# Performance work log

Hardware: AMD Instinct MI355X
Metric: run time of the kernel (lower is better)

The kernel has to match this reference:

```python
import jax, jax.numpy as jnp
import numpy as np

B, S, D, H, F = 64, 512, 1024, 1024, 1024  # note: module requires H == D
EPS = 1e-6


def setup_inputs() -> dict:
    key = jax.random.key(0)
    ks = jax.random.split(key, 14)
    p = lambda k, shape: 0.02 * jax.random.normal(k, shape, dtype=jnp.float32)
    return {
        "hidden_state": jax.random.normal(ks[0], (B, S, D), dtype=jnp.float32),
        "field_hidden_state": jax.random.normal(ks[1], (B, S, F), dtype=jnp.float32),
        "input": jax.random.normal(ks[2], (B, D), dtype=jnp.float32),
        "finished": jnp.zeros((B, 1), dtype=bool),
        "W1": p(ks[3], (H, D)), "b1": p(ks[4], (H,)),
        "W2": p(ks[5], (H, D)), "b2": p(ks[6], (H,)),
        "W3": p(ks[7], (H, 2 * D)), "b3": p(ks[8], (H,)),
        "W4": p(ks[9], (H, F)), "b4": p(ks[10], (H,)),
        "W5": p(ks[11], (H, D)), "b5": p(ks[12], (H,)),
    }


def _norm_over_seq(w):
    # manual exp/max/sum softmax over seq dim (axis 0) with 1e-6 guard, as in torch
    w = jnp.exp(w - jnp.max(w, axis=0, keepdims=True))
    return w / (EPS + jnp.sum(w, axis=0, keepdims=True))


def reference(hidden_state, field_hidden_state, input, finished,
              W1, b1, W2, b2, W3, b3, W4, b4, W5, b5):
    hs = jnp.transpose(hidden_state, (1, 0, 2))        # [S, B, D]
    fs = jnp.transpose(field_hidden_state, (1, 0, 2))  # [S, B, F]
    phi_h = jnp.tanh(hs @ W1.T + b1)                   # [S, B, H]
    phi_f = jnp.tanh(fs @ W4.T + b4)                   # [S, B, H]

    gamma_h = jnp.tanh(input @ W2.T + b2)              # [B, H]
    weights = _norm_over_seq(jnp.sum(phi_h * gamma_h, axis=2, keepdims=True))  # [S, B, 1]

    alpha_h = jnp.tanh(input @ W5.T + b5)              # [B, H]
    field_w = _norm_over_seq(jnp.sum(phi_f * alpha_h, axis=2, keepdims=True))  # [S, B, 1]

    wf = weights * field_w
    weights = wf / (EPS + jnp.sum(wf, axis=0, keepdims=True))  # [S, B, 1]

    context = jnp.sum(hs * weights, axis=0)            # [B, D]
    out = jnp.concatenate([context, input], axis=-1) @ W3.T + b3  # [B, H]
    out = jnp.where(finished, jnp.zeros_like(out), out)
    return out, weights
```

## Files before the change

### kernel.cpp

```cpp
#include <hip/hip_runtime.h>

#define EPS 1e-6f

typedef _Float16 f16;
typedef _Float16 f16x4 __attribute__((ext_vector_type(4)));
typedef _Float16 f16x8 __attribute__((ext_vector_type(8)));
typedef float f32x4 __attribute__((ext_vector_type(4)));

__device__ __forceinline__ float tanh_fast(float x) {
    float e = __expf(2.0f * x);
    return 1.0f - 2.0f / (e + 1.0f);
}

__global__ __launch_bounds__(256) void conv_kernel(
    const float4* __restrict__ src, f16x4* __restrict__ dst, int n4)
{
    int stride = gridDim.x * 256;
    for (int i = blockIdx.x * 256 + threadIdx.x; i < n4; i += stride) {
        float4 v = src[i];
        f16x4 o; o[0]=(f16)v.x; o[1]=(f16)v.y; o[2]=(f16)v.z; o[3]=(f16)v.w;
        dst[i] = o;
    }
}

__global__ __launch_bounds__(256) void gamal_kernel(
    const float* __restrict__ inp,
    const float* __restrict__ W2, const float* __restrict__ b2,
    const float* __restrict__ W5, const float* __restrict__ b5,
    float* __restrict__ gamm, float* __restrict__ alph)
{
    const float* W  = blockIdx.y ? W5 : W2;
    const float* bs = blockIdx.y ? b5 : b2;
    float* dst      = blockIdx.y ? alph : gamm;
    int wid = threadIdx.x >> 6, lane = threadIdx.x & 63;
    int p = blockIdx.x * 4 + wid;
    int b = p >> 10, h = p & 1023;
    const float4* wr = (const float4*)(W + (size_t)h * 1024);
    const float4* xr = (const float4*)(inp + (size_t)b * 1024);
    float acc = 0.f;
    #pragma unroll
    for (int j = 0; j < 4; ++j) {
        float4 w4 = wr[lane + 64 * j];
        float4 x4 = xr[lane + 64 * j];
        acc += w4.x * x4.x + w4.y * x4.y + w4.z * x4.z + w4.w * x4.w;
    }
    #pragma unroll
    for (int o = 32; o; o >>= 1) acc += __shfl_xor(acc, o);
    if (lane == 0) dst[p] = tanh_fast(acc + bs[h]);
}

__global__ __launch_bounds__(256, 4) void gemm_logits_kernel(
    const f16* __restrict__ Ah,
    const f16* __restrict__ Wh,
    const float* __restrict__ b1, const float* __restrict__ b4,
    const float* __restrict__ gamm, const float* __restrict__ alph,
    float* __restrict__ Lpart)
{
    __shared__ __align__(16) char smA[16384];
    __shared__ __align__(16) char smW[16384];
    __shared__ float rowpart[128][2];

    const int lin = blockIdx.x;
    const int gidx = (lin & 7) * 512 + (lin >> 3);
    const int mat = gidx >> 11;
    const int rem = gidx & 2047;
    const int m_blk = rem >> 3;
    const int nc = rem & 7;
    const int m0 = m_blk << 7;
    const int hc0 = nc << 7;
    const int bidx = m_blk >> 2;

    const f16* A   = Ah + (size_t)mat * 33554432;
    const f16* W   = Wh + (size_t)mat * 1048576;
    const float* bv = mat ? b4 : b1;
    const float* gv = mat ? alph : gamm;

    const int t = threadIdx.x;
    const int lane = t & 63;
    const int wv = t >> 6;
    const int wr = wv >> 1;
    const int wc = wv & 1;
    const int c16 = lane & 15;
    const int kg = lane >> 4;

    const int lrow = lane >> 3, lslot = lane & 7;
    const int kchunk = lslot ^ lrow;

    const int swzr = (c16 & 7) << 4;
    const int aoffb = (wr * 64 + c16) * 128;
    const int woffb = (wc * 64 + c16) * 128;
    const int kg16 = kg * 16;

    f32x4 acc[4][4];
    #pragma unroll
    for (int i = 0; i < 4; ++i)
        #pragma unroll
        for (int j = 0; j < 4; ++j) acc[i][j] = (f32x4){0.f, 0.f, 0.f, 0.f};

    for (int kt = 0; kt < 16; ++kt) {
        #pragma unroll
        for (int j = 0; j < 4; ++j) {
            int r = wv * 32 + j * 8;
            const f16* srcA = A + (size_t)(m0 + r + lrow) * 1024 + kt * 64 + kchunk * 8;
            __builtin_amdgcn_global_load_lds(
                (const __attribute__((address_space(1))) void*)srcA,
                (__attribute__((address_space(3))) void*)(smA + r * 128), 16, 0, 0);
        }
        #pragma unroll
        for (int j = 0; j < 4; ++j) {
            int r = wv * 32 + j * 8;
            const f16* srcW = W + (size_t)(hc0 + r + lrow) * 1024 + kt * 64 + kchunk * 8;
            __builtin_amdgcn_global_load_lds(
                (const __attribute__((address_space(1))) void*)srcW,
                (__attribute__((address_space(3))) void*)(smW + r * 128), 16, 0, 0);
        }
        __syncthreads();

        #pragma unroll
        for (int kk = 0; kk < 2; ++kk) {
            const int ko = (kk * 64 + kg16) ^ swzr;
            f16x8 af[4], wf[4];
            #pragma unroll
            for (int i = 0; i < 4; ++i) af[i] = *(const f16x8*)(smA + aoffb + i * 2048 + ko);
            #pragma unroll
            for (int i = 0; i < 4; ++i) wf[i] = *(const f16x8*)(smW + woffb + i * 2048 + ko);
            #pragma unroll
            for (int ni = 0; ni < 4; ++ni)
                #pragma unroll
                for (int mi = 0; mi < 4; ++mi)
                    acc[mi][ni] = __builtin_amdgcn_mfma_f32_16x16x32_f16(af[mi], wf[ni], acc[mi][ni], 0, 0, 0);
        }
        __syncthreads();
    }

    float g[4], bb[4];
    #pragma unroll
    for (int ni = 0; ni < 4; ++ni) {
        int h = hc0 + wc * 64 + ni * 16 + c16;
        g[ni]  = gv[(bidx << 10) + h];
        bb[ni] = bv[h];
    }
    #pragma unroll
    for (int mi = 0; mi < 4; ++mi) {
        #pragma unroll
        for (int q = 0; q < 4; ++q) {
            float v = tanh_fast(acc[mi][0][q] + bb[0]) * g[0]
                    + tanh_fast(acc[mi][1][q] + bb[1]) * g[1]
                    + tanh_fast(acc[mi][2][q] + bb[2]) * g[2]
                    + tanh_fast(acc[mi][3][q] + bb[3]) * g[3];
            v += __shfl_xor(v, 1);
            v += __shfl_xor(v, 2);
            v += __shfl_xor(v, 4);
            v += __shfl_xor(v, 8);
            if (c16 == 0)
                rowpart[wr * 64 + mi * 16 + kg * 4 + q][wc] = v;
        }
    }
    __syncthreads();
    if (t < 128)
        Lpart[(size_t)(mat * 8 + nc) * 32768 + m0 + t] = rowpart[t][0] + rowpart[t][1];
}

__device__ __forceinline__ float blockMax(float v, float* sm) {
    #pragma unroll
    for (int o = 32; o; o >>= 1) v = fmaxf(v, __shfl_xor(v, o));
    if ((threadIdx.x & 63) == 0) sm[threadIdx.x >> 6] = v;
    __syncthreads();
    v = fmaxf(fmaxf(sm[0], sm[1]), fmaxf(sm[2], sm[3]));
    __syncthreads();
    return v;
}
__device__ __forceinline__ float blockSum(float v, float* sm) {
    #pragma unroll
    for (int o = 32; o; o >>= 1) v += __shfl_xor(v, o);
    if ((threadIdx.x & 63) == 0) sm[threadIdx.x >> 6] = v;
    __syncthreads();
    v = sm[0] + sm[1] + sm[2] + sm[3];
    __syncthreads();
    return v;
}

__global__ __launch_bounds__(256) void softmax_combine_kernel(
    const float* __restrict__ Lp,
    float* __restrict__ wfin, float* __restrict__ dout)
{
    __shared__ float sm[4];
    int b = blockIdx.x, t = threadIdx.x;
    float h0 = 0.f, h1 = 0.f, f0 = 0.f, f1 = 0.f;
    #pragma unroll
    for (int nc = 0; nc < 8; ++nc) {
        h0 += Lp[nc * 32768 + b * 512 + t];
        h1 += Lp[nc * 32768 + b * 512 + 256 + t];
        f0 += Lp[(8 + nc) * 32768 + b * 512 + t];
        f1 += Lp[(8 + nc) * 32768 + b * 512 + 256 + t];
    }
    float mh = blockMax(fmaxf(h0, h1), sm);
    float mf = blockMax(fmaxf(f0, f1), sm);
    float e0 = __expf(h0 - mh), e1 = __expf(h1 - mh);
    float q0 = __expf(f0 - mf), q1 = __expf(f1 - mf);
    float sh = blockSum(e0 + e1, sm);
    float sf = blockSum(q0 + q1, sm);
    float wh0 = e0 / (EPS + sh), wh1 = e1 / (EPS + sh);
    float wq0 = q0 / (EPS + sf), wq1 = q1 / (EPS + sf);
    float c0 = wh0 * wq0, c1 = wh1 * wq1;
    float sc = blockSum(c0 + c1, sm);
    float r0 = c0 / (EPS + sc), r1 = c1 / (EPS + sc);
    wfin[b * 512 + t]       = r0;
    wfin[b * 512 + 256 + t] = r1;
    dout[65536 + t * 64 + b]         = r0;
    dout[65536 + (256 + t) * 64 + b] = r1;
}

__global__ __launch_bounds__(256) void context_kernel(
    const f16* __restrict__ Ah, const float* __restrict__ wgt,
    float* __restrict__ ctxpart)
{
    int dq = blockIdx.x;
    int b  = blockIdx.y;
    int sh = blockIdx.z;
    int t = threadIdx.x;
    int ss = t >> 6, ds = t & 63;
    __shared__ float part[4][64][8];
    float a[8] = {0,0,0,0,0,0,0,0};
    int sBase = sh * 256 + ss * 64;
    const f16* hp = Ah + (size_t)b * 524288 + dq * 512 + ds * 8;
    for (int i = 0; i < 64; ++i) {
        int s = sBase + i;
        float w = wgt[b * 512 + s];
        f16x8 v = *(const f16x8*)(hp + (size_t)s * 1024);
        #pragma unroll
        for (int j = 0; j < 8; ++j) a[j] += w * (float)v[j];
    }
    #pragma unroll
    for (int j = 0; j < 8; ++j) part[ss][ds][j] = a[j];
    __syncthreads();
    if (ss == 0) {
        #pragma unroll
        for (int j = 0; j < 8; ++j) {
            float o = part[0][ds][j] + part[1][ds][j] + part[2][ds][j] + part[3][ds][j];
            ctxpart[(size_t)sh * 65536 + b * 1024 + dq * 512 + ds * 8 + j] = o;
        }
    }
}

__global__ __launch_bounds__(256) void out_kernel(
    const float* __restrict__ ctxpart, const float* __restrict__ inp,
    const float* __restrict__ W3, const float* __restrict__ b3,
    const unsigned char* __restrict__ fin, float* __restrict__ out)
{
    int t = threadIdx.x, wid = t >> 6, lane = t & 63;
    int h = blockIdx.x * 4 + wid;
    __shared__ __align__(16) float xs[2048];
    float4* xsv = (float4*)xs;
    float4 wreg[8];
    const float4* w3r = (const float4*)(W3 + (size_t)h * 2048);
    #pragma unroll
    for (int j = 0; j < 8; ++j) wreg[j] = w3r[lane + 64 * j];
    const float4* cp = (const float4*)ctxpart;
    const float4* xp = (const float4*)inp;
    for (int b = 0; b < 64; ++b) {
        __syncthreads();
        {
            float4 c0 = cp[b * 256 + t];
            float4 c1 = cp[16384 + b * 256 + t];
            float4 cc; cc.x = c0.x + c1.x; cc.y = c0.y + c1.y;
            cc.z = c0.z + c1.z; cc.w = c0.w + c1.w;
            xsv[t] = cc;
            xsv[256 + t] = xp[b * 256 + t];
        }
        __syncthreads();
        float acc = 0.f;
        #pragma unroll
        for (int j = 0; j < 8; ++j) {
            float4 x = xsv[lane + 64 * j];
            acc += wreg[j].x * x.x + wreg[j].y * x.y + wreg[j].z * x.z + wreg[j].w * x.w;
        }
        #pragma unroll
        for (int o = 32; o; o >>= 1) acc += __shfl_xor(acc, o);
        if (lane == 0) out[b * 1024 + h] = fin[b] ? 0.f : (acc + b3[h]);
    }
}

extern "C" void kernel_launch(void* const* d_in, const int* in_sizes, int n_in,
                              void* d_out, int out_size, void* d_ws, size_t ws_size,
                              hipStream_t stream)
{
    const float* hidden = (const float*)d_in[0];
    const float* field  = (const float*)d_in[1];
    const float* input  = (const float*)d_in[2];
    const unsigned char* fin = (const unsigned char*)d_in[3];
    const float* W1 = (const float*)d_in[4];
    const float* b1 = (const float*)d_in[5];
    const float* W2 = (const float*)d_in[6];
    const float* b2 = (const float*)d_in[7];
    const float* W3 = (const float*)d_in[8];
    const float* b3 = (const float*)d_in[9];
    const float* W4 = (const float*)d_in[10];
    const float* b4 = (const float*)d_in[11];
    const float* W5 = (const float*)d_in[12];
    const float* b5 = (const float*)d_in[13];
    float* out = (float*)d_out;

    char* ws = (char*)d_ws;
    float* Lpart = (float*)(ws);
    float* wfin  = (float*)(ws + 2097152);
    float* gamm  = (float*)(ws + 2228224);
    float* alph  = (float*)(ws + 2490368);
    float* ctxp  = (float*)(ws + 2752512);
    f16*   Wh    = (f16*)(ws + 3276800);
    f16*   Ah    = (f16*)(ws + 7471104);

    conv_kernel<<<4096, 256, 0, stream>>>((const float4*)hidden, (f16x4*)Ah, 8388608);
    conv_kernel<<<4096, 256, 0, stream>>>((const float4*)field,  (f16x4*)(Ah + 33554432), 8388608);
    conv_kernel<<<1024, 256, 0, stream>>>((const float4*)W1, (f16x4*)Wh, 262144);
    conv_kernel<<<1024, 256, 0, stream>>>((const float4*)W4, (f16x4*)(Wh + 1048576), 262144);

    gamal_kernel<<<dim3(16384, 2), 256, 0, stream>>>(input, W2, b2, W5, b5, gamm, alph);
    gemm_logits_kernel<<<4096, 256, 0, stream>>>(Ah, Wh, b1, b4, gamm, alph, Lpart);
    softmax_combine_kernel<<<64, 256, 0, stream>>>(Lpart, wfin, out);
    context_kernel<<<dim3(2, 64, 2), 256, 0, stream>>>(Ah, wfin, ctxp);
    out_kernel<<<256, 256, 0, stream>>>(ctxp, input, W3, b3, fin, out);
}
```

Baseline: 344.3 us.

## Rework logits GEMM into 256x256 tiles with double-buffered phased LDS pipeline

The logits GEMM moves from 128x128 tiles with 4 waves to 256x256 tiles with 8 waves, using double-buffered LDS (128 KB) and a four-phase schedule. Each phase issues global-to-LDS loads for the next k-tile while running MFMAs on the current one, separated by raw s_barrier, sched_barrier and setprio hints. The larger tile halves the number of column-chunk partials written and summed by the softmax kernel, and raises operand reuse per LDS byte. The costs are occupancy limited to one block per CU, heavy register pressure from 32 accumulators, and fragile manual vmcnt accounting.

```diff
diff --git a/kernel.cpp b/kernel.cpp
--- a/kernel.cpp
+++ b/kernel.cpp
@@ -6,6 +6,10 @@
 typedef _Float16 f16x4 __attribute__((ext_vector_type(4)));
 typedef _Float16 f16x8 __attribute__((ext_vector_type(8)));
 typedef float f32x4 __attribute__((ext_vector_type(4)));
+
+#define PHASE_BAR() do { __builtin_amdgcn_sched_barrier(0); \
+                         __builtin_amdgcn_s_barrier();      \
+                         __builtin_amdgcn_sched_barrier(0); } while (0)
 
 __device__ __forceinline__ float tanh_fast(float x) {
     float e = __expf(2.0f * x);
@@ -49,37 +53,37 @@
     if (lane == 0) dst[p] = tanh_fast(acc + bs[h]);
 }
 
-__global__ __launch_bounds__(256, 4) void gemm_logits_kernel(
+__global__ __launch_bounds__(512, 1) void gemm_logits_kernel(
     const f16* __restrict__ Ah,
     const f16* __restrict__ Wh,
     const float* __restrict__ b1, const float* __restrict__ b4,
     const float* __restrict__ gamm, const float* __restrict__ alph,
     float* __restrict__ Lpart)
 {
-    __shared__ __align__(16) char smA[16384];
-    __shared__ __align__(16) char smW[16384];
-    __shared__ float rowpart[128][2];
+    __shared__ __align__(16) char smA[2][32768];
+    __shared__ __align__(16) char smW[2][32768];
+    __shared__ float rowpart[256][4];
 
     const int lin = blockIdx.x;
-    const int gidx = (lin & 7) * 512 + (lin >> 3);
-    const int mat = gidx >> 11;
-    const int rem = gidx & 2047;
-    const int m_blk = rem >> 3;
-    const int nc = rem & 7;
-    const int m0 = m_blk << 7;
-    const int hc0 = nc << 7;
-    const int bidx = m_blk >> 2;
-
-    const f16* A   = Ah + (size_t)mat * 33554432;
-    const f16* W   = Wh + (size_t)mat * 1048576;
+    const int swz = (lin & 7) * 128 + (lin >> 3);
+    const int mat = swz >> 9;
+    const int rem = swz & 511;
+    const int m_blk = rem >> 2;
+    const int nc = rem & 3;
+    const int m0 = m_blk << 8;
+    const int hc0 = nc << 8;
+    const int bidx = m_blk >> 1;
+
+    const f16* A = Ah + (size_t)mat * 33554432;
+    const f16* W = Wh + (size_t)mat * 1048576;
     const float* bv = mat ? b4 : b1;
     const float* gv = mat ? alph : gamm;
 
     const int t = threadIdx.x;
     const int lane = t & 63;
     const int wv = t >> 6;
-    const int wr = wv >> 1;
-    const int wc = wv & 1;
+    const int wr = wv >> 2;
+    const int wc = wv & 3;
     const int c16 = lane & 15;
     const int kg = lane >> 4;
 
@@ -87,50 +91,126 @@
     const int kchunk = lslot ^ lrow;
 
     const int swzr = (c16 & 7) << 4;
-    const int aoffb = (wr * 64 + c16) * 128;
+    const int aoffb = (wr * 128 + c16) * 128;
     const int woffb = (wc * 64 + c16) * 128;
     const int kg16 = kg * 16;
 
-    f32x4 acc[4][4];
-    #pragma unroll
-    for (int i = 0; i < 4; ++i)
+    f32x4 acc[8][4];
+    #pragma unroll
+    for (int i = 0; i < 8; ++i)
         #pragma unroll
         for (int j = 0; j < 4; ++j) acc[i][j] = (f32x4){0.f, 0.f, 0.f, 0.f};
 
+    auto stageA = [&](int kt, char* buf, int h) {
+        #pragma unroll
+        for (int j = 0; j < 2; ++j) {
+            int q = wv * 2 + j;
+            int r = (q >> 3) * 128 + h * 64 + (q & 7) * 8;
+            const f16* src = A + (size_t)(m0 + r + lrow) * 1024 + kt * 64 + kchunk * 8;
+            __builtin_amdgcn_global_load_lds(
+                (const __attribute__((address_space(1))) void*)src,
+                (__attribute__((address_space(3))) void*)(buf + r * 128), 16, 0, 0);
+        }
+    };
+    auto stageW = [&](int kt, char* buf, int h) {
+        #pragma unroll
+        for (int j = 0; j < 2; ++j) {
+            int q = wv * 2 + j;
+            int r = (q >> 2) * 64 + h * 32 + (q & 3) * 8;
+            const f16* src = W + (size_t)(hc0 + r + lrow) * 1024 + kt * 64 + kchunk * 8;
+            __builtin_amdgcn_global_load_lds(
+                (const __attribute__((address_space(1))) void*)src,
+                (__attribute__((address_space(3))) void*)(buf + r * 128), 16, 0, 0);
+        }
+    };
+
+    stageA(0, smA[0], 0); stageA(0, smA[0], 1);
+    stageW(0, smW[0], 0); stageW(0, smW[0], 1);
+    stageA(1, smA[1], 0);
+    __builtin_amdgcn_sched_barrier(0);
+    asm volatile("s_waitcnt vmcnt(2)" ::: "memory");
+    PHASE_BAR();
+
     for (int kt = 0; kt < 16; ++kt) {
-        #pragma unroll
-        for (int j = 0; j < 4; ++j) {
-            int r = wv * 32 + j * 8;
-            const f16* srcA = A + (size_t)(m0 + r + lrow) * 1024 + kt * 64 + kchunk * 8;
-            __builtin_amdgcn_global_load_lds(
-                (const __attribute__((address_space(1))) void*)srcA,
-                (__attribute__((address_space(3))) void*)(smA + r * 128), 16, 0, 0);
-        }
-        #pragma unroll
-        for (int j = 0; j < 4; ++j) {
-            int r = wv * 32 + j * 8;
-            const f16* srcW = W + (size_t)(hc0 + r + lrow) * 1024 + kt * 64 + kchunk * 8;
-            __builtin_amdgcn_global_load_lds(
-                (const __attribute__((address_space(1))) void*)srcW,
-                (__attribute__((address_space(3))) void*)(smW + r * 128), 16, 0, 0);
-        }
-        __syncthreads();
-
-        #pragma unroll
-        for (int kk = 0; kk < 2; ++kk) {
-            const int ko = (kk * 64 + kg16) ^ swzr;
-            f16x8 af[4], wf[4];
-            #pragma unroll
-            for (int i = 0; i < 4; ++i) af[i] = *(const f16x8*)(smA + aoffb + i * 2048 + ko);
-            #pragma unroll
-            for (int i = 0; i < 4; ++i) wf[i] = *(const f16x8*)(smW + woffb + i * 2048 + ko);
-            #pragma unroll
-            for (int ni = 0; ni < 4; ++ni)
+        char* aC = smA[kt & 1];
+        char* wC = smW[kt & 1];
+        char* aN = smA[(kt & 1) ^ 1];
+        char* wN = smW[(kt & 1) ^ 1];
+        const int kt1 = kt < 15 ? kt + 1 : 15;
+        const int kt2 = kt < 14 ? kt + 2 : 15;
+
+        f16x8 af[8], bf0[4], bf1[4];
+
+        stageA(kt1, aN, 1);
+        #pragma unroll
+        for (int mi = 0; mi < 4; ++mi)
+            #pragma unroll
+            for (int kk = 0; kk < 2; ++kk)
+                af[mi * 2 + kk] = *(const f16x8*)(aC + aoffb + mi * 2048 + ((kk * 64 + kg16) ^ swzr));
+        #pragma unroll
+        for (int ni = 0; ni < 2; ++ni)
+            #pragma unroll
+            for (int kk = 0; kk < 2; ++kk)
+                bf0[ni * 2 + kk] = *(const f16x8*)(wC + woffb + ni * 2048 + ((kk * 64 + kg16) ^ swzr));
+        __builtin_amdgcn_s_setprio(1);
+        #pragma unroll
+        for (int ni = 0; ni < 2; ++ni)
+            #pragma unroll
+            for (int mi = 0; mi < 4; ++mi)
                 #pragma unroll
-                for (int mi = 0; mi < 4; ++mi)
-                    acc[mi][ni] = __builtin_amdgcn_mfma_f32_16x16x32_f16(af[mi], wf[ni], acc[mi][ni], 0, 0, 0);
-        }
-        __syncthreads();
+                for (int kk = 0; kk < 2; ++kk)
+                    acc[mi][ni] = __builtin_amdgcn_mfma_f32_16x16x32_f16(af[mi * 2 + kk], bf0[ni * 2 + kk], acc[mi][ni], 0, 0, 0);
+        __builtin_amdgcn_s_setprio(0);
+        PHASE_BAR();
+
+        stageW(kt1, wN, 0);
+        #pragma unroll
+        for (int ni = 0; ni < 2; ++ni)
+            #pragma unroll
+            for (int kk = 0; kk < 2; ++kk)
+                bf1[ni * 2 + kk] = *(const f16x8*)(wC + woffb + 4096 + ni * 2048 + ((kk * 64 + kg16) ^ swzr));
+        __builtin_amdgcn_s_setprio(1);
+        #pragma unroll
+        for (int ni = 0; ni < 2; ++ni)
+            #pragma unroll
+            for (int mi = 0; mi < 4; ++mi)
+                #pragma unroll
+                for (int kk = 0; kk < 2; ++kk)
+                    acc[mi][ni + 2] = __builtin_amdgcn_mfma_f32_16x16x32_f16(af[mi * 2 + kk], bf1[ni * 2 + kk], acc[mi][ni + 2], 0, 0, 0);
+        __builtin_amdgcn_s_setprio(0);
+        PHASE_BAR();
+
+        stageW(kt1, wN, 1);
+        #pragma unroll
+        for (int mi = 0; mi < 4; ++mi)
+            #pragma unroll
+            for (int kk = 0; kk < 2; ++kk)
+                af[mi * 2 + kk] = *(const f16x8*)(aC + aoffb + 8192 + mi * 2048 + ((kk * 64 + kg16) ^ swzr));
+        __builtin_amdgcn_s_setprio(1);
+        #pragma unroll
+        for (int ni = 0; ni < 2; ++ni)
+            #pragma unroll
+            for (int mi = 0; mi < 4; ++mi)
+                #pragma unroll
+                for (int kk = 0; kk < 2; ++kk)
+                    acc[mi + 4][ni] = __builtin_amdgcn_mfma_f32_16x16x32_f16(af[mi * 2 + kk], bf0[ni * 2 + kk], acc[mi + 4][ni], 0, 0, 0);
+        __builtin_amdgcn_s_setprio(0);
+        PHASE_BAR();
+
+        stageA(kt2, aC, 0);
+        __builtin_amdgcn_sched_barrier(0);
+        __builtin_amdgcn_s_setprio(1);
+        #pragma unroll
+        for (int ni = 0; ni < 2; ++ni)
+            #pragma unroll
+            for (int mi = 0; mi < 4; ++mi)
+                #pragma unroll
+                for (int kk = 0; kk < 2; ++kk)
+                    acc[mi + 4][ni + 2] = __builtin_amdgcn_mfma_f32_16x16x32_f16(af[mi * 2 + kk], bf1[ni * 2 + kk], acc[mi + 4][ni + 2], 0, 0, 0);
+        __builtin_amdgcn_s_setprio(0);
+        __builtin_amdgcn_sched_barrier(0);
+        asm volatile("s_waitcnt vmcnt(2)" ::: "memory");
+        PHASE_BAR();
     }
 
     float g[4], bb[4];
@@ -141,7 +221,7 @@
         bb[ni] = bv[h];
     }
     #pragma unroll
-    for (int mi = 0; mi < 4; ++mi) {
+    for (int mi = 0; mi < 8; ++mi) {
         #pragma unroll
         for (int q = 0; q < 4; ++q) {
             float v = tanh_fast(acc[mi][0][q] + bb[0]) * g[0]
@@ -153,12 +233,13 @@
             v += __shfl_xor(v, 4);
             v += __shfl_xor(v, 8);
             if (c16 == 0)
-                rowpart[wr * 64 + mi * 16 + kg * 4 + q][wc] = v;
-        }
-    }
-    __syncthreads();
-    if (t < 128)
-        Lpart[(size_t)(mat * 8 + nc) * 32768 + m0 + t] = rowpart[t][0] + rowpart[t][1];
+                rowpart[wr * 128 + mi * 16 + kg * 4 + q][wc] = v;
+        }
+    }
+    __syncthreads();
+    if (t < 256)
+        Lpart[(size_t)(mat * 4 + nc) * 32768 + m0 + t] =
+            rowpart[t][0] + rowpart[t][1] + rowpart[t][2] + rowpart[t][3];
 }
 
 __device__ __forceinline__ float blockMax(float v, float* sm) {
@@ -188,11 +269,11 @@
     int b = blockIdx.x, t = threadIdx.x;
     float h0 = 0.f, h1 = 0.f, f0 = 0.f, f1 = 0.f;
     #pragma unroll
-    for (int nc = 0; nc < 8; ++nc) {
+    for (int nc = 0; nc < 4; ++nc) {
         h0 += Lp[nc * 32768 + b * 512 + t];
         h1 += Lp[nc * 32768 + b * 512 + 256 + t];
-        f0 += Lp[(8 + nc) * 32768 + b * 512 + t];
-        f1 += Lp[(8 + nc) * 32768 + b * 512 + 256 + t];
+        f0 += Lp[(4 + nc) * 32768 + b * 512 + t];
+        f1 += Lp[(4 + nc) * 32768 + b * 512 + 256 + t];
     }
     float mh = blockMax(fmaxf(h0, h1), sm);
     float mf = blockMax(fmaxf(f0, f1), sm);
@@ -316,7 +397,7 @@
     conv_kernel<<<1024, 256, 0, stream>>>((const float4*)W4, (f16x4*)(Wh + 1048576), 262144);
 
     gamal_kernel<<<dim3(16384, 2), 256, 0, stream>>>(input, W2, b2, W5, b5, gamm, alph);
-    gemm_logits_kernel<<<4096, 256, 0, stream>>>(Ah, Wh, b1, b4, gamm, alph, Lpart);
+    gemm_logits_kernel<<<1024, 512, 0, stream>>>(Ah, Wh, b1, b4, gamm, alph, Lpart);
     softmax_combine_kernel<<<64, 256, 0, stream>>>(Lpart, wfin, out);
     context_kernel<<<dim3(2, 64, 2), 256, 0, stream>>>(Ah, wfin, ctxp);
     out_kernel<<<256, 256, 0, stream>>>(ctxp, input, W3, b3, fin, out);
```

New measurement: 365.3 us. 1.06x slower.

## Widen logits GEMM tile to 128x256 and fuse fp16 conversion launches

Applied to the files above, without the earlier changes.

Merges the four fp32-to-fp16 conversion launches into one grid-stride kernel that picks its source buffer by index range. The logits GEMM tile grows from 128x128 to 128x256, so each wave holds 4x8 accumulators, the A tile is reloaded half as often, and only 4 N-chunk partials are written, with the softmax reduction updated to match. In exchange the kernel uses more registers and LDS, and its launch bound drops from 4 to 2 blocks per CU, which lowers occupancy and latency hiding.

```diff
diff --git a/kernel.cpp b/kernel.cpp
--- a/kernel.cpp
+++ b/kernel.cpp
@@ -12,14 +12,22 @@
     return 1.0f - 2.0f / (e + 1.0f);
 }
 
-__global__ __launch_bounds__(256) void conv_kernel(
-    const float4* __restrict__ src, f16x4* __restrict__ dst, int n4)
-{
-    int stride = gridDim.x * 256;
-    for (int i = blockIdx.x * 256 + threadIdx.x; i < n4; i += stride) {
-        float4 v = src[i];
+__global__ __launch_bounds__(256) void convall_kernel(
+    const float4* __restrict__ hidden, const float4* __restrict__ field,
+    const float4* __restrict__ W1, const float4* __restrict__ W4,
+    f16x4* __restrict__ Ah, f16x4* __restrict__ Af,
+    f16x4* __restrict__ Wh1, f16x4* __restrict__ Wh4)
+{
+    const int stride = gridDim.x * 256;
+    for (int i = blockIdx.x * 256 + threadIdx.x; i < 17301504; i += stride) {
+        const float4* s; f16x4* d; int off;
+        if (i < 8388608)       { s = hidden; d = Ah;  off = i; }
+        else if (i < 16777216) { s = field;  d = Af;  off = i - 8388608; }
+        else if (i < 17039360) { s = W1;     d = Wh1; off = i - 16777216; }
+        else                   { s = W4;     d = Wh4; off = i - 17039360; }
+        float4 v = s[off];
         f16x4 o; o[0]=(f16)v.x; o[1]=(f16)v.y; o[2]=(f16)v.z; o[3]=(f16)v.w;
-        dst[i] = o;
+        d[off] = o;
     }
 }
 
@@ -49,7 +57,7 @@
     if (lane == 0) dst[p] = tanh_fast(acc + bs[h]);
 }
 
-__global__ __launch_bounds__(256, 4) void gemm_logits_kernel(
+__global__ __launch_bounds__(256, 2) void gemm_logits_kernel(
     const f16* __restrict__ Ah,
     const f16* __restrict__ Wh,
     const float* __restrict__ b1, const float* __restrict__ b4,
@@ -57,21 +65,21 @@
     float* __restrict__ Lpart)
 {
     __shared__ __align__(16) char smA[16384];
-    __shared__ __align__(16) char smW[16384];
+    __shared__ __align__(16) char smW[32768];
     __shared__ float rowpart[128][2];
 
     const int lin = blockIdx.x;
-    const int gidx = (lin & 7) * 512 + (lin >> 3);
-    const int mat = gidx >> 11;
-    const int rem = gidx & 2047;
-    const int m_blk = rem >> 3;
-    const int nc = rem & 7;
+    const int swz = (lin & 7) * 256 + (lin >> 3);
+    const int mat = swz >> 10;
+    const int rem = swz & 1023;
+    const int m_blk = rem >> 2;
+    const int nc = rem & 3;
     const int m0 = m_blk << 7;
-    const int hc0 = nc << 7;
+    const int hc0 = nc << 8;
     const int bidx = m_blk >> 2;
 
-    const f16* A   = Ah + (size_t)mat * 33554432;
-    const f16* W   = Wh + (size_t)mat * 1048576;
+    const f16* A = Ah + (size_t)mat * 33554432;
+    const f16* W = Wh + (size_t)mat * 1048576;
     const float* bv = mat ? b4 : b1;
     const float* gv = mat ? alph : gamm;
 
@@ -88,14 +96,14 @@
 
     const int swzr = (c16 & 7) << 4;
     const int aoffb = (wr * 64 + c16) * 128;
-    const int woffb = (wc * 64 + c16) * 128;
+    const int woffb = (wc * 128 + c16) * 128;
     const int kg16 = kg * 16;
 
-    f32x4 acc[4][4];
+    f32x4 acc[4][8];
     #pragma unroll
     for (int i = 0; i < 4; ++i)
         #pragma unroll
-        for (int j = 0; j < 4; ++j) acc[i][j] = (f32x4){0.f, 0.f, 0.f, 0.f};
+        for (int j = 0; j < 8; ++j) acc[i][j] = (f32x4){0.f, 0.f, 0.f, 0.f};
 
     for (int kt = 0; kt < 16; ++kt) {
         #pragma unroll
@@ -107,8 +115,8 @@
                 (__attribute__((address_space(3))) void*)(smA + r * 128), 16, 0, 0);
         }
         #pragma unroll
-        for (int j = 0; j < 4; ++j) {
-            int r = wv * 32 + j * 8;
+        for (int j = 0; j < 8; ++j) {
+            int r = wv * 64 + j * 8;
             const f16* srcW = W + (size_t)(hc0 + r + lrow) * 1024 + kt * 64 + kchunk * 8;
             __builtin_amdgcn_global_load_lds(
                 (const __attribute__((address_space(1))) void*)srcW,
@@ -119,13 +127,13 @@
         #pragma unroll
         for (int kk = 0; kk < 2; ++kk) {
             const int ko = (kk * 64 + kg16) ^ swzr;
-            f16x8 af[4], wf[4];
+            f16x8 af[4], wf[8];
             #pragma unroll
             for (int i = 0; i < 4; ++i) af[i] = *(const f16x8*)(smA + aoffb + i * 2048 + ko);
             #pragma unroll
-            for (int i = 0; i < 4; ++i) wf[i] = *(const f16x8*)(smW + woffb + i * 2048 + ko);
+            for (int i = 0; i < 8; ++i) wf[i] = *(const f16x8*)(smW + woffb + i * 2048 + ko);
             #pragma unroll
-            for (int ni = 0; ni < 4; ++ni)
+            for (int ni = 0; ni < 8; ++ni)
                 #pragma unroll
                 for (int mi = 0; mi < 4; ++mi)
                     acc[mi][ni] = __builtin_amdgcn_mfma_f32_16x16x32_f16(af[mi], wf[ni], acc[mi][ni], 0, 0, 0);
@@ -133,10 +141,10 @@
         __syncthreads();
     }
 
-    float g[4], bb[4];
-    #pragma unroll
-    for (int ni = 0; ni < 4; ++ni) {
-        int h = hc0 + wc * 64 + ni * 16 + c16;
+    float g[8], bb[8];
+    #pragma unroll
+    for (int ni = 0; ni < 8; ++ni) {
+        int h = hc0 + wc * 128 + ni * 16 + c16;
         g[ni]  = gv[(bidx << 10) + h];
         bb[ni] = bv[h];
     }
@@ -144,10 +152,10 @@
     for (int mi = 0; mi < 4; ++mi) {
         #pragma unroll
         for (int q = 0; q < 4; ++q) {
-            float v = tanh_fast(acc[mi][0][q] + bb[0]) * g[0]
-                    + tanh_fast(acc[mi][1][q] + bb[1]) * g[1]
-                    + tanh_fast(acc[mi][2][q] + bb[2]) * g[2]
-                    + tanh_fast(acc[mi][3][q] + bb[3]) * g[3];
+            float v = 0.f;
+            #pragma unroll
+            for (int ni = 0; ni < 8; ++ni)
+                v += tanh_fast(acc[mi][ni][q] + bb[ni]) * g[ni];
             v += __shfl_xor(v, 1);
             v += __shfl_xor(v, 2);
             v += __shfl_xor(v, 4);
@@ -158,7 +166,7 @@
     }
     __syncthreads();
     if (t < 128)
-        Lpart[(size_t)(mat * 8 + nc) * 32768 + m0 + t] = rowpart[t][0] + rowpart[t][1];
+        Lpart[(size_t)(mat * 4 + nc) * 32768 + m0 + t] = rowpart[t][0] + rowpart[t][1];
 }
 
 __device__ __forceinline__ float blockMax(float v, float* sm) {
@@ -188,11 +196,11 @@
     int b = blockIdx.x, t = threadIdx.x;
     float h0 = 0.f, h1 = 0.f, f0 = 0.f, f1 = 0.f;
     #pragma unroll
-    for (int nc = 0; nc < 8; ++nc) {
+    for (int nc = 0; nc < 4; ++nc) {
         h0 += Lp[nc * 32768 + b * 512 + t];
         h1 += Lp[nc * 32768 + b * 512 + 256 + t];
-        f0 += Lp[(8 + nc) * 32768 + b * 512 + t];
-        f1 += Lp[(8 + nc) * 32768 + b * 512 + 256 + t];
+        f0 += Lp[(4 + nc) * 32768 + b * 512 + t];
+        f1 += Lp[(4 + nc) * 32768 + b * 512 + 256 + t];
     }
     float mh = blockMax(fmaxf(h0, h1), sm);
     float mf = blockMax(fmaxf(f0, f1), sm);
@@ -310,13 +318,14 @@
     f16*   Wh    = (f16*)(ws + 3276800);
     f16*   Ah    = (f16*)(ws + 7471104);
 
-    conv_kernel<<<4096, 256, 0, stream>>>((const float4*)hidden, (f16x4*)Ah, 8388608);
-    conv_kernel<<<4096, 256, 0, stream>>>((const float4*)field,  (f16x4*)(Ah + 33554432), 8388608);
-    conv_kernel<<<1024, 256, 0, stream>>>((const float4*)W1, (f16x4*)Wh, 262144);
-    conv_kernel<<<1024, 256, 0, stream>>>((const float4*)W4, (f16x4*)(Wh + 1048576), 262144);
+    convall_kernel<<<8192, 256, 0, stream>>>(
+        (const float4*)hidden, (const float4*)field,
+        (const float4*)W1, (const float4*)W4,
+        (f16x4*)Ah, (f16x4*)(Ah + 33554432),
+        (f16x4*)Wh, (f16x4*)(Wh + 1048576));
 
     gamal_kernel<<<dim3(16384, 2), 256, 0, stream>>>(input, W2, b2, W5, b5, gamm, alph);
-    gemm_logits_kernel<<<4096, 256, 0, stream>>>(Ah, Wh, b1, b4, gamm, alph, Lpart);
+    gemm_logits_kernel<<<2048, 256, 0, stream>>>(Ah, Wh, b1, b4, gamm, alph, Lpart);
     softmax_combine_kernel<<<64, 256, 0, stream>>>(Lpart, wfin, out);
     context_kernel<<<dim3(2, 64, 2), 256, 0, stream>>>(Ah, wfin, ctxp);
     out_kernel<<<256, 256, 0, stream>>>(ctxp, input, W3, b3, fin, out);
```

Result: faster. 327.8 us (-4.8%).

## Fuse fp32-to-fp16 activation conversion into GEMM A-tile loading

Applied to the files above, without the earlier changes.

Drops the separate conversion passes over hidden and field states. The logits GEMM now loads fp32 activations into registers, converts them with packed round-toward-zero conversion and writes them swizzled into LDS, prefetching the next K tile. The context kernel reads fp32 hidden directly. The gamma/alpha kernel reuses each weight row across 8 batch rows, and the weight conversions are merged into one launch. This removes a large extra write and read of the activations, at the cost of more register pressure (occupancy hint lowered to 3) and doubled global read bytes for A inside the GEMM.

```diff
diff --git a/kernel.cpp b/kernel.cpp
--- a/kernel.cpp
+++ b/kernel.cpp
@@ -3,6 +3,7 @@
 #define EPS 1e-6f
 
 typedef _Float16 f16;
+typedef __fp16 h16x2 __attribute__((ext_vector_type(2)));
 typedef _Float16 f16x4 __attribute__((ext_vector_type(4)));
 typedef _Float16 f16x8 __attribute__((ext_vector_type(8)));
 typedef float f32x4 __attribute__((ext_vector_type(4)));
@@ -12,14 +13,18 @@
     return 1.0f - 2.0f / (e + 1.0f);
 }
 
-__global__ __launch_bounds__(256) void conv_kernel(
-    const float4* __restrict__ src, f16x4* __restrict__ dst, int n4)
-{
-    int stride = gridDim.x * 256;
-    for (int i = blockIdx.x * 256 + threadIdx.x; i < n4; i += stride) {
-        float4 v = src[i];
+__global__ __launch_bounds__(256) void convw_kernel(
+    const float4* __restrict__ W1, const float4* __restrict__ W4,
+    f16x4* __restrict__ Wh1, f16x4* __restrict__ Wh4)
+{
+    const int stride = gridDim.x * 256;
+    for (int i = blockIdx.x * 256 + threadIdx.x; i < 524288; i += stride) {
+        const float4* s = (i < 262144) ? W1 : W4;
+        f16x4* d       = (i < 262144) ? Wh1 : Wh4;
+        int off = i & 262143;
+        float4 v = s[off];
         f16x4 o; o[0]=(f16)v.x; o[1]=(f16)v.y; o[2]=(f16)v.z; o[3]=(f16)v.w;
-        dst[i] = o;
+        d[off] = o;
     }
 }
 
@@ -33,24 +38,31 @@
     const float* bs = blockIdx.y ? b5 : b2;
     float* dst      = blockIdx.y ? alph : gamm;
     int wid = threadIdx.x >> 6, lane = threadIdx.x & 63;
-    int p = blockIdx.x * 4 + wid;
-    int b = p >> 10, h = p & 1023;
+    int hb = blockIdx.x >> 3;
+    int bb = blockIdx.x & 7;
+    int h = hb * 4 + wid;
+    int b0 = bb * 8;
     const float4* wr = (const float4*)(W + (size_t)h * 1024);
-    const float4* xr = (const float4*)(inp + (size_t)b * 1024);
-    float acc = 0.f;
-    #pragma unroll
-    for (int j = 0; j < 4; ++j) {
-        float4 w4 = wr[lane + 64 * j];
-        float4 x4 = xr[lane + 64 * j];
-        acc += w4.x * x4.x + w4.y * x4.y + w4.z * x4.z + w4.w * x4.w;
-    }
-    #pragma unroll
-    for (int o = 32; o; o >>= 1) acc += __shfl_xor(acc, o);
-    if (lane == 0) dst[p] = tanh_fast(acc + bs[h]);
-}
-
-__global__ __launch_bounds__(256, 4) void gemm_logits_kernel(
-    const f16* __restrict__ Ah,
+    float4 wreg[4];
+    #pragma unroll
+    for (int j = 0; j < 4; ++j) wreg[j] = wr[lane + 64 * j];
+    float bias = bs[h];
+    for (int b = b0; b < b0 + 8; ++b) {
+        const float4* xr = (const float4*)(inp + (size_t)b * 1024);
+        float acc = 0.f;
+        #pragma unroll
+        for (int j = 0; j < 4; ++j) {
+            float4 x4 = xr[lane + 64 * j];
+            acc += wreg[j].x * x4.x + wreg[j].y * x4.y + wreg[j].z * x4.z + wreg[j].w * x4.w;
+        }
+        #pragma unroll
+        for (int o = 32; o; o >>= 1) acc += __shfl_xor(acc, o);
+        if (lane == 0) dst[b * 1024 + h] = tanh_fast(acc + bias);
+    }
+}
+
+__global__ __launch_bounds__(256, 3) void gemm_logits_kernel(
+    const float* __restrict__ Ahid, const float* __restrict__ Afld,
     const f16* __restrict__ Wh,
     const float* __restrict__ b1, const float* __restrict__ b4,
     const float* __restrict__ gamm, const float* __restrict__ alph,
@@ -70,8 +82,8 @@
     const int hc0 = nc << 7;
     const int bidx = m_blk >> 2;
 
-    const f16* A   = Ah + (size_t)mat * 33554432;
-    const f16* W   = Wh + (size_t)mat * 1048576;
+    const float* A = mat ? Afld : Ahid;
+    const f16*  W  = Wh + (size_t)mat * 1048576;
     const float* bv = mat ? b4 : b1;
     const float* gv = mat ? alph : gamm;
 
@@ -83,6 +95,10 @@
     const int c16 = lane & 15;
     const int kg = lane >> 4;
 
+    const int srow = t >> 1;
+    const int shalf = t & 1;
+    const float* aRow = A + (size_t)(m0 + srow) * 1024 + shalf * 32;
+
     const int lrow = lane >> 3, lslot = lane & 7;
     const int kchunk = lslot ^ lrow;
 
@@ -97,15 +113,28 @@
         #pragma unroll
         for (int j = 0; j < 4; ++j) acc[i][j] = (f32x4){0.f, 0.f, 0.f, 0.f};
 
-    for (int kt = 0; kt < 16; ++kt) {
+    float4 a_ld[8];
+    auto loadA = [&](int kt) {
+        const float4* ap = (const float4*)(aRow + kt * 64);
+        #pragma unroll
+        for (int j = 0; j < 8; ++j) a_ld[j] = ap[j];
+    };
+    auto writeA = [&]() {
+        char* ad = smA + srow * 128;
+        const int swzw = (srow & 7) << 4;
+        const int wb = shalf * 64;
         #pragma unroll
         for (int j = 0; j < 4; ++j) {
-            int r = wv * 32 + j * 8;
-            const f16* srcA = A + (size_t)(m0 + r + lrow) * 1024 + kt * 64 + kchunk * 8;
-            __builtin_amdgcn_global_load_lds(
-                (const __attribute__((address_space(1))) void*)srcA,
-                (__attribute__((address_space(3))) void*)(smA + r * 128), 16, 0, 0);
-        }
+            union { f16x8 v; h16x2 q[4]; } u;
+            float4 x = a_ld[2 * j], y = a_ld[2 * j + 1];
+            u.q[0] = __builtin_amdgcn_cvt_pkrtz(x.x, x.y);
+            u.q[1] = __builtin_amdgcn_cvt_pkrtz(x.z, x.w);
+            u.q[2] = __builtin_amdgcn_cvt_pkrtz(y.x, y.y);
+            u.q[3] = __builtin_amdgcn_cvt_pkrtz(y.z, y.w);
+            *(f16x8*)(ad + ((wb + j * 16) ^ swzw)) = u.v;
+        }
+    };
+    auto gloadW = [&](int kt) {
         #pragma unroll
         for (int j = 0; j < 4; ++j) {
             int r = wv * 32 + j * 8;
@@ -114,7 +143,14 @@
                 (const __attribute__((address_space(1))) void*)srcW,
                 (__attribute__((address_space(3))) void*)(smW + r * 128), 16, 0, 0);
         }
+    };
+
+    loadA(0);
+    for (int kt = 0; kt < 16; ++kt) {
+        gloadW(kt);
+        writeA();
         __syncthreads();
+        loadA(kt < 15 ? kt + 1 : 15);
 
         #pragma unroll
         for (int kk = 0; kk < 2; ++kk) {
@@ -212,7 +248,7 @@
 }
 
 __global__ __launch_bounds__(256) void context_kernel(
-    const f16* __restrict__ Ah, const float* __restrict__ wgt,
+    const float* __restrict__ hs, const float* __restrict__ wgt,
     float* __restrict__ ctxpart)
 {
     int dq = blockIdx.x;
@@ -220,26 +256,27 @@
     int sh = blockIdx.z;
     int t = threadIdx.x;
     int ss = t >> 6, ds = t & 63;
-    __shared__ float part[4][64][8];
-    float a[8] = {0,0,0,0,0,0,0,0};
+    __shared__ float4 part[4][64];
+    const float4* hp = (const float4*)hs;
+    float ax = 0.f, ay = 0.f, az = 0.f, aw = 0.f;
     int sBase = sh * 256 + ss * 64;
-    const f16* hp = Ah + (size_t)b * 524288 + dq * 512 + ds * 8;
     for (int i = 0; i < 64; ++i) {
         int s = sBase + i;
         float w = wgt[b * 512 + s];
-        f16x8 v = *(const f16x8*)(hp + (size_t)s * 1024);
-        #pragma unroll
-        for (int j = 0; j < 8; ++j) a[j] += w * (float)v[j];
-    }
-    #pragma unroll
-    for (int j = 0; j < 8; ++j) part[ss][ds][j] = a[j];
+        float4 v = hp[(size_t)(b * 512 + s) * 256 + dq * 64 + ds];
+        ax += v.x * w; ay += v.y * w; az += v.z * w; aw += v.w * w;
+    }
+    float4 r; r.x = ax; r.y = ay; r.z = az; r.w = aw;
+    part[ss][ds] = r;
     __syncthreads();
     if (ss == 0) {
-        #pragma unroll
-        for (int j = 0; j < 8; ++j) {
-            float o = part[0][ds][j] + part[1][ds][j] + part[2][ds][j] + part[3][ds][j];
-            ctxpart[(size_t)sh * 65536 + b * 1024 + dq * 512 + ds * 8 + j] = o;
-        }
+        float4 a0 = part[0][ds], a1 = part[1][ds], a2 = part[2][ds], a3 = part[3][ds];
+        float4 o;
+        o.x = a0.x + a1.x + a2.x + a3.x;
+        o.y = a0.y + a1.y + a2.y + a3.y;
+        o.z = a0.z + a1.z + a2.z + a3.z;
+        o.w = a0.w + a1.w + a2.w + a3.w;
+        ((float4*)ctxpart)[(size_t)sh * 16384 + b * 256 + dq * 64 + ds] = o;
     }
 }
 
@@ -308,16 +345,14 @@
     float* alph  = (float*)(ws + 2490368);
     float* ctxp  = (float*)(ws + 2752512);
     f16*   Wh    = (f16*)(ws + 3276800);
-    f16*   Ah    = (f16*)(ws + 7471104);
-
-    conv_kernel<<<4096, 256, 0, stream>>>((const float4*)hidden, (f16x4*)Ah, 8388608);
-    conv_kernel<<<4096, 256, 0, stream>>>((const float4*)field,  (f16x4*)(Ah + 33554432), 8388608);
-    conv_kernel<<<1024, 256, 0, stream>>>((const float4*)W1, (f16x4*)Wh, 262144);
-    conv_kernel<<<1024, 256, 0, stream>>>((const float4*)W4, (f16x4*)(Wh + 1048576), 262144);
-
-    gamal_kernel<<<dim3(16384, 2), 256, 0, stream>>>(input, W2, b2, W5, b5, gamm, alph);
-    gemm_logits_kernel<<<4096, 256, 0, stream>>>(Ah, Wh, b1, b4, gamm, alph, Lpart);
+
+    convw_kernel<<<512, 256, 0, stream>>>(
+        (const float4*)W1, (const float4*)W4,
+        (f16x4*)Wh, (f16x4*)(Wh + 1048576));
+
+    gamal_kernel<<<dim3(2048, 2), 256, 0, stream>>>(input, W2, b2, W5, b5, gamm, alph);
+    gemm_logits_kernel<<<4096, 256, 0, stream>>>(hidden, field, Wh, b1, b4, gamm, alph, Lpart);
     softmax_combine_kernel<<<64, 256, 0, stream>>>(Lpart, wfin, out);
-    context_kernel<<<dim3(2, 64, 2), 256, 0, stream>>>(Ah, wfin, ctxp);
+    context_kernel<<<dim3(4, 64, 2), 256, 0, stream>>>(hidden, wfin, ctxp);
     out_kernel<<<256, 256, 0, stream>>>(ctxp, input, W3, b3, fin, out);
 }
```

Result: slower. 446.2 us (+29.6%).
